# Performance work log

Measured on AMD Instinct MI355X. Metric: run time of the kernel, lower is better.

## Reference

```python
import jax, jax.numpy as jnp
import numpy as np

N_NODES = 100000
N_EDGES = 1600000
IN_CH = 64
HID = 64
OUT = 2


def sage_conv(x, src, dst, W_agg, W_root, b):
    # PyG SAGEConv (mean aggr): out = lin_l(mean_{j in N(i)} x_j) + lin_r(x_i)
    n = x.shape[0]
    msgs = x[src]                                        # [E, F] gather
    agg = jax.ops.segment_sum(msgs, dst, num_segments=n)  # [N, F] scatter-add
    cnt = jax.ops.segment_sum(jnp.ones((src.shape[0], 1), x.dtype), dst, num_segments=n)
    agg = agg / jnp.maximum(cnt, 1)                      # mean; isolated nodes -> 0
    return agg @ W_agg + x @ W_root + b


def setup_inputs() -> dict:
    key = jax.random.key(0)
    ks = jax.random.split(key, 8)
    s = lambda f: 1.0 / np.sqrt(f)
    x = jax.random.normal(ks[0], (N_NODES, IN_CH), dtype=jnp.float32)
    edge_index = jax.random.randint(ks[1], (2, N_EDGES), 0, N_NODES, dtype=jnp.int64)
    return {
        "x": x,
        "edge_index": edge_index,
        "W1_agg": jax.random.normal(ks[2], (IN_CH, HID), dtype=jnp.float32) * s(IN_CH),
        "W1_root": jax.random.normal(ks[3], (IN_CH, HID), dtype=jnp.float32) * s(IN_CH),
        "b1": jnp.zeros((HID,), jnp.float32),
        "W2_agg": jax.random.normal(ks[4], (HID, HID), dtype=jnp.float32) * s(HID),
        "W2_root": jax.random.normal(ks[5], (HID, HID), dtype=jnp.float32) * s(HID),
        "b2": jnp.zeros((HID,), jnp.float32),
        "W_lin": jax.random.normal(ks[6], (HID, OUT), dtype=jnp.float32) * s(HID),
        "b_lin": jnp.zeros((OUT,), jnp.float32),
    }


def reference(x, edge_index, W1_agg, W1_root, b1, W2_agg, W2_root, b2, W_lin, b_lin):
    src, dst = edge_index[0], edge_index[1]
    h = jax.nn.relu(sage_conv(x, src, dst, W1_agg, W1_root, b1))   # dropout = identity (eval)
    h = jax.nn.relu(sage_conv(h, src, dst, W2_agg, W2_root, b2))
    return h @ W_lin + b_lin
```

## Files before the change

kernel.cpp:

```cpp
#include <hip/hip_runtime.h>
#include <hip/hip_bf16.h>

#define FEAT 64
#define CHUNK 8192
#define MAX_NB 1024

typedef __attribute__((ext_vector_type(8))) short bf16x8;
typedef __attribute__((ext_vector_type(4))) float f32x4;
typedef __attribute__((ext_vector_type(2))) float f32x2;

__device__ __forceinline__ float bflo2f(unsigned int u) {
    union { unsigned int u; float f; } v; v.u = u << 16; return v.f;
}
__device__ __forceinline__ float bfhi2f(unsigned int u) {
    union { unsigned int u; float f; } v; v.u = u & 0xffff0000u; return v.f;
}
__device__ __forceinline__ unsigned short f2bf(float f) {
    union { float f; unsigned int u; } v; v.f = f;
    unsigned int u = v.u;
    u += 0x7fffu + ((u >> 16) & 1u);
    return (unsigned short)(u >> 16);
}
__device__ __forceinline__ f32x2 bfpair(unsigned int u) {
    f32x2 r; r.x = bflo2f(u & 0xffffu); r.y = bfhi2f(u); return r;
}

__global__ __launch_bounds__(256) void prep_kernel(
    const unsigned short* __restrict__ xh, const int* __restrict__ ei32,
    const void* __restrict__ w1a, const void* __restrict__ w1r,
    const void* __restrict__ b1,  const void* __restrict__ w2a,
    const void* __restrict__ w2r, const void* __restrict__ b2,
    const void* __restrict__ wl,  const void* __restrict__ bl,
    float* __restrict__ wbuf, unsigned short* __restrict__ Wt,
    int* __restrict__ flags, const void* __restrict__ x_in,
    unsigned short* __restrict__ x16, int n8) {
    __shared__ int cnt_bf, cnt_nz;
    int tid = threadIdx.x;
    if (tid == 0) { cnt_bf = 0; cnt_nz = 0; }
    __syncthreads();
    unsigned short h = xh[tid * 2];
    int e = (h >> 7) & 0xFF;
    if (e >= 110 && e <= 132) atomicAdd(&cnt_bf, 1);
    if (ei32[tid * 2 + 1] != 0) atomicAdd(&cnt_nz, 1);
    __syncthreads();
    int f0 = (cnt_bf >= 128) ? 1 : 0;
    if (blockIdx.x == 0 && tid == 0) {
        flags[0] = f0;
        flags[1] = (cnt_nz < 8) ? 1 : 0;
    }
    int i = blockIdx.x * 256 + tid;
    if (i < 16642) {
        const void* src; int off;
        if      (i < 4096)  { src = w1a; off = i; }
        else if (i < 8192)  { src = w1r; off = i - 4096; }
        else if (i < 8256)  { src = b1;  off = i - 8192; }
        else if (i < 12352) { src = w2a; off = i - 8256; }
        else if (i < 16448) { src = w2r; off = i - 12352; }
        else if (i < 16512) { src = b2;  off = i - 16448; }
        else if (i < 16640) { src = wl;  off = i - 16512; }
        else                { src = bl;  off = i - 16640; }
        float v = f0 ? bflo2f(((const unsigned short*)src)[off])
                     : ((const float*)src)[off];
        wbuf[i] = v;
        unsigned short hv = f2bf(v);
        if (i < 4096)                      Wt[(off & 63) * 128 + (off >> 6)] = hv;
        else if (i < 8192)                 Wt[(off & 63) * 128 + 64 + (off >> 6)] = hv;
        else if (i >= 8256 && i < 12352)   Wt[8192 + (off & 63) * 128 + (off >> 6)] = hv;
        else if (i >= 12352 && i < 16448)  Wt[8192 + (off & 63) * 128 + 64 + (off >> 6)] = hv;
    }
    if (!f0 && i < n8) {
        float4 a = ((const float4*)x_in)[2 * i];
        float4 b = ((const float4*)x_in)[2 * i + 1];
        uint4 o;
        o.x = (unsigned int)f2bf(a.x) | ((unsigned int)f2bf(a.y) << 16);
        o.y = (unsigned int)f2bf(a.z) | ((unsigned int)f2bf(a.w) << 16);
        o.z = (unsigned int)f2bf(b.x) | ((unsigned int)f2bf(b.y) << 16);
        o.w = (unsigned int)f2bf(b.z) | ((unsigned int)f2bf(b.w) << 16);
        ((uint4*)x16)[i] = o;
    }
}

__global__ __launch_bounds__(256) void p1_hist_kernel(
    const int* __restrict__ ei32, int* __restrict__ hist,
    int E, int N, int NB, int EC, const int* __restrict__ flags) {
    __shared__ int lh[MAX_NB];
    int tid = threadIdx.x, c = blockIdx.x;
    for (int i = tid; i < NB; i += 256) lh[i] = 0;
    __syncthreads();
    int idx64 = flags[1];
    long base = (long)c * CHUNK;
#pragma unroll 4
    for (int j = 0; j < CHUNK / 256; ++j) {
        long e = base + j * 256 + tid;
        if (e < E) {
            int d = idx64 ? ei32[2 * ((long)E + e)] : ei32[(long)E + e];
            if ((unsigned)d < (unsigned)N)
                atomicAdd(&lh[d >> 8], 1);
        }
    }
    __syncthreads();
    for (int k = tid; k < NB; k += 256) hist[(long)k * EC + c] = lh[k];
}

__global__ __launch_bounds__(256) void scan1_kernel(const int* __restrict__ in,
                                                    int* __restrict__ out,
                                                    int* __restrict__ blocksum, int n) {
    int tid = threadIdx.x;
    int base = blockIdx.x * 2048 + tid * 8;
    int v[8];
    int tsum = 0;
#pragma unroll
    for (int i = 0; i < 8; ++i) {
        v[i] = (base + i < n) ? in[base + i] : 0;
        tsum += v[i];
    }
    int lane = tid & 63;
    int x = tsum;
#pragma unroll
    for (int off = 1; off < 64; off <<= 1) {
        int y = __shfl_up(x, off);
        if (lane >= off) x += y;
    }
    __shared__ int wsum[4];
    int wave = tid >> 6;
    if (lane == 63) wsum[wave] = x;
    __syncthreads();
    int woff = 0;
#pragma unroll
    for (int w = 0; w < 4; ++w) if (w < wave) woff += wsum[w];
    int run = woff + x - tsum;
#pragma unroll
    for (int i = 0; i < 8; ++i) {
        if (base + i < n) out[base + i] = run;
        run += v[i];
    }
    if (tid == 255) blocksum[blockIdx.x] = woff + x;
}

__global__ void scan3_kernel(int* __restrict__ out, const int* __restrict__ blocksum, int n) {
    int i = blockIdx.x * 256 + threadIdx.x;
    if (i >= n) return;
    int nb = i >> 11;
    int pre = 0;
    for (int b = 0; b < nb; ++b) pre += blocksum[b];
    out[i] += pre;
}

__global__ __launch_bounds__(256) void p3_scatter_kernel(
    const int* __restrict__ ei32, const int* __restrict__ hscan,
    int* __restrict__ bkt, int E, int N, int NB, int EC,
    const int* __restrict__ flags) {
    __shared__ int lh[MAX_NB];
    int tid = threadIdx.x, c = blockIdx.x;
    for (int i = tid; i < NB; i += 256) lh[i] = 0;
    __syncthreads();
    int idx64 = flags[1];
    long base = (long)c * CHUNK;
#pragma unroll 4
    for (int j = 0; j < CHUNK / 256; ++j) {
        long e = base + j * 256 + tid;
        if (e < E) {
            int s = idx64 ? ei32[2 * e]             : ei32[e];
            int d = idx64 ? ei32[2 * ((long)E + e)] : ei32[(long)E + e];
            if ((unsigned)d < (unsigned)N) {
                if ((unsigned)s >= (unsigned)N) s = 0;
                int k = d >> 8;
                int r = atomicAdd(&lh[k], 1);
                bkt[hscan[(long)k * EC + c] + r] = s | ((d & 255) << 20);
            }
        }
    }
}

__global__ __launch_bounds__(256) void p4_build_kernel(
    const int* __restrict__ bkt, const int* __restrict__ hscan, const int* __restrict__ hist,
    int* __restrict__ offs, int* __restrict__ cnt, int* __restrict__ srcs,
    int E, int N, int NB, int EC) {
    int k = blockIdx.x, tid = threadIdx.x;
    int start = hscan[(long)k * EC];
    int end = (k + 1 < NB) ? hscan[(long)(k + 1) * EC]
                           : (hscan[(long)NB * EC - 1] + hist[(long)NB * EC - 1]);
    __shared__ int lc[256], lheads[256], wsum[4];
    lc[tid] = 0;
    __syncthreads();
    for (int e = start + tid; e < end; e += 256)
        atomicAdd(&lc[(bkt[e] >> 20) & 255], 1);
    __syncthreads();
    int cv = lc[tid];
    int lane = tid & 63, wave = tid >> 6;
    int x = cv;
#pragma unroll
    for (int off = 1; off < 64; off <<= 1) {
        int y = __shfl_up(x, off);
        if (lane >= off) x += y;
    }
    if (lane == 63) wsum[wave] = x;
    __syncthreads();
    int woff = 0;
#pragma unroll
    for (int w = 0; w < 4; ++w) if (w < wave) woff += wsum[w];
    int excl = woff + x - cv;
    int gnode = k * 256 + tid;
    if (gnode < N) { offs[gnode] = start + excl; cnt[gnode] = cv; }
    lheads[tid] = excl;
    __syncthreads();
    for (int e = start + tid; e < end; e += 256) {
        int p = bkt[e];
        int d8 = (p >> 20) & 255;
        int pos = start + atomicAdd(&lheads[d8], 1);
        srcs[pos] = p & 0xFFFFF;
    }
}

__global__ __launch_bounds__(256) void aggregate_kernel(
    const void* __restrict__ feat_raw, const unsigned short* __restrict__ feat_ws,
    const int* __restrict__ srcs,
    const int* __restrict__ offs, const int* __restrict__ cnt,
    unsigned short* __restrict__ agg16, int N, const int* __restrict__ flags) {
    const unsigned short* feat16 = flags[0] ? (const unsigned short*)feat_raw : feat_ws;
    int tid = threadIdx.x;
    int lane = tid & 63;
    int wave = tid >> 6;
    int g = lane >> 3;
    int li = lane & 7;
    int node = (blockIdx.x * 4 + wave) * 8 + g;
    if (node >= N) return;
    int start = offs[node];
    int deg = cnt[node];
    f32x2 a0 = {0.f, 0.f}, a1 = a0, a2 = a0, a3 = a0;
    int j = 0;
    for (; j + 4 <= deg; j += 4) {
        int s0 = srcs[start + j];
        int s1 = srcs[start + j + 1];
        int s2 = srcs[start + j + 2];
        int s3 = srcs[start + j + 3];
        uint4 u0 = *(const uint4*)(feat16 + (size_t)s0 * FEAT + 8 * li);
        uint4 u1 = *(const uint4*)(feat16 + (size_t)s1 * FEAT + 8 * li);
        uint4 u2 = *(const uint4*)(feat16 + (size_t)s2 * FEAT + 8 * li);
        uint4 u3 = *(const uint4*)(feat16 + (size_t)s3 * FEAT + 8 * li);
        a0 += bfpair(u0.x); a1 += bfpair(u0.y); a2 += bfpair(u0.z); a3 += bfpair(u0.w);
        a0 += bfpair(u1.x); a1 += bfpair(u1.y); a2 += bfpair(u1.z); a3 += bfpair(u1.w);
        a0 += bfpair(u2.x); a1 += bfpair(u2.y); a2 += bfpair(u2.z); a3 += bfpair(u2.w);
        a0 += bfpair(u3.x); a1 += bfpair(u3.y); a2 += bfpair(u3.z); a3 += bfpair(u3.w);
    }
    for (; j < deg; ++j) {
        int s = srcs[start + j];
        uint4 u = *(const uint4*)(feat16 + (size_t)s * FEAT + 8 * li);
        a0 += bfpair(u.x); a1 += bfpair(u.y); a2 += bfpair(u.z); a3 += bfpair(u.w);
    }
    float inv = 1.0f / (float)(deg > 0 ? deg : 1);
    uint4 o;
    o.x = (unsigned)f2bf(a0.x * inv) | ((unsigned)f2bf(a0.y * inv) << 16);
    o.y = (unsigned)f2bf(a1.x * inv) | ((unsigned)f2bf(a1.y * inv) << 16);
    o.z = (unsigned)f2bf(a2.x * inv) | ((unsigned)f2bf(a2.y * inv) << 16);
    o.w = (unsigned)f2bf(a3.x * inv) | ((unsigned)f2bf(a3.y * inv) << 16);
    *(uint4*)(agg16 + (size_t)node * FEAT + 8 * li) = o;
}

__global__ __launch_bounds__(256) void sage_gemm_kernel(
    const unsigned short* __restrict__ agg16,
    const void* __restrict__ root_raw, const unsigned short* __restrict__ root_ws,
    const unsigned short* __restrict__ Wt, const float* __restrict__ bias,
    unsigned short* __restrict__ out16, int N,
    const float* __restrict__ wl, const float* __restrict__ bl,
    void* __restrict__ out_final, const int* __restrict__ flags, int root_sel) {

    const unsigned short* root16 =
        (root_sel && !flags[0]) ? root_ws : (const unsigned short*)root_raw;

    __shared__ unsigned short A_l[64][136];
    __shared__ unsigned short B_l[64][136];

    int tid = threadIdx.x;
    int blk = blockIdx.x;

#pragma unroll
    for (int i = 0; i < 4; ++i) {
        int ch = tid + i * 256;
        int n = ch >> 4, kc = ch & 15;
        *(uint4*)&B_l[n][kc * 8] = *(const uint4*)(Wt + n * 128 + kc * 8);
    }
#pragma unroll
    for (int i = 0; i < 4; ++i) {
        int ch = tid + i * 256;
        int r = ch >> 4, c = ch & 15;
        int row = blk * 64 + r;
        uint4 u = make_uint4(0, 0, 0, 0);
        if (row < N)
            u = (c < 8) ? ((const uint4*)(agg16 + (size_t)row * FEAT))[c]
                        : ((const uint4*)(root16 + (size_t)row * FEAT))[c - 8];
        *(uint4*)&A_l[r][c * 8] = u;
    }
    __syncthreads();

    int lane = tid & 63;
    int wave = tid >> 6;
    int r0 = wave * 16;
    int m = lane & 15, quad = lane >> 4;

    f32x4 acc0 = {0.f, 0.f, 0.f, 0.f};
    f32x4 acc1 = acc0, acc2 = acc0, acc3 = acc0;

#pragma unroll
    for (int k0 = 0; k0 < 128; k0 += 32) {
        bf16x8 a = *(const bf16x8*)&A_l[r0 + m][k0 + quad * 8];
        bf16x8 b0 = *(const bf16x8*)&B_l[ 0 + m][k0 + quad * 8];
        bf16x8 b1 = *(const bf16x8*)&B_l[16 + m][k0 + quad * 8];
        bf16x8 b2 = *(const bf16x8*)&B_l[32 + m][k0 + quad * 8];
        bf16x8 b3 = *(const bf16x8*)&B_l[48 + m][k0 + quad * 8];
        acc0 = __builtin_amdgcn_mfma_f32_16x16x32_bf16(a, b0, acc0, 0, 0, 0);
        acc1 = __builtin_amdgcn_mfma_f32_16x16x32_bf16(a, b1, acc1, 0, 0, 0);
        acc2 = __builtin_amdgcn_mfma_f32_16x16x32_bf16(a, b2, acc2, 0, 0, 0);
        acc3 = __builtin_amdgcn_mfma_f32_16x16x32_bf16(a, b3, acc3, 0, 0, 0);
    }
    __syncthreads();

#pragma unroll
    for (int c = 0; c < 4; ++c) {
        f32x4 av = (c == 0) ? acc0 : (c == 1) ? acc1 : (c == 2) ? acc2 : acc3;
        float bv = bias[c * 16 + m];
#pragma unroll
        for (int reg = 0; reg < 4; ++reg) {
            float v = fmaxf(av[reg] + bv, 0.f);
            A_l[r0 + quad * 4 + reg][c * 16 + m] = f2bf(v);
        }
    }
    __syncthreads();

#pragma unroll
    for (int i = 0; i < 2; ++i) {
        int ch = tid + i * 256;
        int r = ch >> 3, c = ch & 7;
        int row = blk * 64 + r;
        if (row < N)
            ((uint4*)(out16 + (size_t)row * FEAT))[c] = *(const uint4*)&A_l[r][c * 8];
    }

    if (wl) {
        int r = tid >> 2, part = tid & 3;
        int row = blk * 64 + r;
        if (row < N) {
            float p0 = 0.f, p1 = 0.f;
#pragma unroll
            for (int j = 0; j < 16; ++j) {
                int f = part * 16 + j;
                float v = bflo2f(A_l[r][f]);
                p0 += v * wl[f * 2 + 0];
                p1 += v * wl[f * 2 + 1];
            }
            p0 += __shfl_down(p0, 2, 4); p0 += __shfl_down(p0, 1, 4);
            p1 += __shfl_down(p1, 2, 4); p1 += __shfl_down(p1, 1, 4);
            if (part == 0) {
                p0 += bl[0];
                p1 += bl[1];
                if (flags[0]) {
                    unsigned int o = ((unsigned int)f2bf(p1) << 16) | (unsigned int)f2bf(p0);
                    ((unsigned int*)out_final)[row] = o;
                } else {
                    ((float2*)out_final)[row] = make_float2(p0, p1);
                }
            }
        }
    }
}

extern "C" void kernel_launch(void* const* d_in, const int* in_sizes, int n_in,
                              void* d_out, int out_size, void* d_ws, size_t ws_size,
                              hipStream_t stream) {
    const void* x_in = d_in[0];
    const int*  ei32 = (const int*)d_in[1];

    int N = in_sizes[0] / FEAT;
    int E = in_sizes[1] / 2;
    int NB = (N + 255) >> 8;
    int EC = (E + CHUNK - 1) / CHUNK;
    int HN = NB * EC;

    unsigned short* x16   = (unsigned short*)d_ws;
    unsigned short* h16   = x16 + (size_t)N * FEAT;
    unsigned short* agg16 = h16 + (size_t)N * FEAT;
    unsigned short* Wt    = agg16 + (size_t)N * FEAT;
    float*          wbuf  = (float*)(Wt + 16384);
    int*            hist  = (int*)(wbuf + 16704);
    int*            hscan = hist + HN;
    int*            bsum  = hscan + HN;
    int*            flags = bsum + 1024;
    int*            offs  = flags + 16;
    int*            cnt   = offs + N;
    int*            bkt   = cnt + N;
    int*            srcs  = bkt + E;

    float* b1_32 = wbuf + 8192;
    float* b2_32 = wbuf + 16448;
    float* wl32  = wbuf + 16512;
    float* bl32  = wbuf + 16640;

    int n8 = N * FEAT / 8;
    int pBlocks = (n8 + 255) / 256;
    if (pBlocks < 66) pBlocks = 66;
    prep_kernel<<<pBlocks, 256, 0, stream>>>(
        (const unsigned short*)x_in, ei32,
        d_in[2], d_in[3], d_in[4], d_in[5], d_in[6], d_in[7], d_in[8], d_in[9],
        wbuf, Wt, flags, x_in, x16, n8);

    p1_hist_kernel<<<EC, 256, 0, stream>>>(ei32, hist, E, N, NB, EC, flags);
    int sB = (HN + 2047) / 2048;
    scan1_kernel<<<sB, 256, 0, stream>>>(hist, hscan, bsum, HN);
    scan3_kernel<<<(HN + 255) / 256, 256, 0, stream>>>(hscan, bsum, HN);
    p3_scatter_kernel<<<EC, 256, 0, stream>>>(ei32, hscan, bkt, E, N, NB, EC, flags);
    p4_build_kernel<<<NB, 256, 0, stream>>>(bkt, hscan, hist, offs, cnt, srcs, E, N, NB, EC);

    int aBlocks = (N + 31) / 32;
    int gBlocks = (N + 63) / 64;

    aggregate_kernel<<<aBlocks, 256, 0, stream>>>(x_in, x16, srcs, offs, cnt, agg16, N, flags);
    sage_gemm_kernel<<<gBlocks, 256, 0, stream>>>(agg16, x_in, x16, Wt, b1_32, h16, N,
                                                  nullptr, nullptr, nullptr, flags, 1);

    aggregate_kernel<<<aBlocks, 256, 0, stream>>>(h16, h16, srcs, offs, cnt, agg16, N, flags);
    sage_gemm_kernel<<<gBlocks, 256, 0, stream>>>(agg16, h16, h16, Wt + 8192, b2_32, h16, N,
                                                  wl32, bl32, d_out, flags, 0);
}
```

Measured before the change: 236.2 us.

## Fuse CSR build stages into one cooperative kernel with grid syncs

Replaces the six separate preprocessing launches (prep, histogram, two scans, scatter, build) with a single cooperative kernel that separates the phases with grid.sync(), falling back to the old launch sequence if the cooperative launch fails. It also halves the edge chunk size so more blocks share the histogram and scatter work, and skips writing the layer-2 hidden features since only the final linear output is needed. This targets per-launch overhead and small-grid tail effects, at the cost of running the scan and build phases on a grid capped at 512 blocks, which adds grid-wide barrier cost and less parallelism in the per-bucket build.

Measured after the change: 488.2 us. +106.7%, slower.

```diff
diff --git a/kernel.cpp b/kernel.cpp
--- a/kernel.cpp
+++ b/kernel.cpp
@@ -1,8 +1,11 @@
 #include <hip/hip_runtime.h>
 #include <hip/hip_bf16.h>
+#include <hip/hip_cooperative_groups.h>
+
+namespace cg = cooperative_groups;
 
 #define FEAT 64
-#define CHUNK 8192
+#define CHUNK 4096
 #define MAX_NB 1024
 
 typedef __attribute__((ext_vector_type(8))) short bf16x8;
@@ -23,6 +26,199 @@
 }
 __device__ __forceinline__ f32x2 bfpair(unsigned int u) {
     f32x2 r; r.x = bflo2f(u & 0xffffu); r.y = bfhi2f(u); return r;
+}
+
+__device__ __forceinline__ void weights_cvt_elem(
+    int i, int f0,
+    const void* w1a, const void* w1r, const void* b1, const void* w2a,
+    const void* w2r, const void* b2, const void* wl, const void* bl,
+    float* wbuf, unsigned short* Wt) {
+    const void* src; int off;
+    if      (i < 4096)  { src = w1a; off = i; }
+    else if (i < 8192)  { src = w1r; off = i - 4096; }
+    else if (i < 8256)  { src = b1;  off = i - 8192; }
+    else if (i < 12352) { src = w2a; off = i - 8256; }
+    else if (i < 16448) { src = w2r; off = i - 12352; }
+    else if (i < 16512) { src = b2;  off = i - 16448; }
+    else if (i < 16640) { src = wl;  off = i - 16512; }
+    else                { src = bl;  off = i - 16640; }
+    float v = f0 ? bflo2f(((const unsigned short*)src)[off])
+                 : ((const float*)src)[off];
+    wbuf[i] = v;
+    unsigned short hv = f2bf(v);
+    if (i < 4096)                      Wt[(off & 63) * 128 + (off >> 6)] = hv;
+    else if (i < 8192)                 Wt[(off & 63) * 128 + 64 + (off >> 6)] = hv;
+    else if (i >= 8256 && i < 12352)   Wt[8192 + (off & 63) * 128 + (off >> 6)] = hv;
+    else if (i >= 12352 && i < 16448)  Wt[8192 + (off & 63) * 128 + 64 + (off >> 6)] = hv;
+}
+
+__global__ __launch_bounds__(256) void coop_build_kernel(
+    const int* __restrict__ ei32, const void* __restrict__ x_in,
+    unsigned short* __restrict__ x16, int n8,
+    const void* __restrict__ w1a, const void* __restrict__ w1r,
+    const void* __restrict__ b1,  const void* __restrict__ w2a,
+    const void* __restrict__ w2r, const void* __restrict__ b2,
+    const void* __restrict__ wl,  const void* __restrict__ bl,
+    float* __restrict__ wbuf, unsigned short* __restrict__ Wt,
+    int* __restrict__ flags,
+    int* __restrict__ hist, int* __restrict__ hscan, int* __restrict__ bsum,
+    int* __restrict__ offs, int* __restrict__ cnt,
+    int* __restrict__ bkt, int* __restrict__ srcs,
+    int E, int N, int NB, int EC, int HN, int sB) {
+
+    cg::grid_group grid = cg::this_grid();
+    __shared__ int lh[MAX_NB];
+    __shared__ int lc[256], lheads[256], wsum[4];
+    __shared__ int s_cnt[2];
+
+    int tid = threadIdx.x;
+    int lane = tid & 63, wave = tid >> 6;
+
+    if (tid == 0) { s_cnt[0] = 0; s_cnt[1] = 0; }
+    __syncthreads();
+    {
+        const unsigned short* xh = (const unsigned short*)x_in;
+        unsigned short h = xh[tid * 2];
+        int e = (h >> 7) & 0xFF;
+        if (e >= 110 && e <= 132) atomicAdd(&s_cnt[0], 1);
+        if (ei32[tid * 2 + 1] != 0) atomicAdd(&s_cnt[1], 1);
+    }
+    __syncthreads();
+    int f0    = (s_cnt[0] >= 128) ? 1 : 0;
+    int idx64 = (s_cnt[1] < 8) ? 1 : 0;
+    if (blockIdx.x == 0 && tid == 0) { flags[0] = f0; flags[1] = idx64; }
+
+    for (int i = blockIdx.x * 256 + tid; i < 16642; i += gridDim.x * 256)
+        weights_cvt_elem(i, f0, w1a, w1r, b1, w2a, w2r, b2, wl, bl, wbuf, Wt);
+
+    if (!f0) {
+        for (int i = blockIdx.x * 256 + tid; i < n8; i += gridDim.x * 256) {
+            float4 a = ((const float4*)x_in)[2 * i];
+            float4 b = ((const float4*)x_in)[2 * i + 1];
+            uint4 o;
+            o.x = (unsigned int)f2bf(a.x) | ((unsigned int)f2bf(a.y) << 16);
+            o.y = (unsigned int)f2bf(a.z) | ((unsigned int)f2bf(a.w) << 16);
+            o.z = (unsigned int)f2bf(b.x) | ((unsigned int)f2bf(b.y) << 16);
+            o.w = (unsigned int)f2bf(b.z) | ((unsigned int)f2bf(b.w) << 16);
+            ((uint4*)x16)[i] = o;
+        }
+    }
+    grid.sync();
+
+    for (int c = blockIdx.x; c < EC; c += gridDim.x) {
+        for (int i = tid; i < NB; i += 256) lh[i] = 0;
+        __syncthreads();
+        long base = (long)c * CHUNK;
+#pragma unroll 4
+        for (int j = 0; j < CHUNK / 256; ++j) {
+            long e = base + j * 256 + tid;
+            if (e < E) {
+                int d = idx64 ? ei32[2 * ((long)E + e)] : ei32[(long)E + e];
+                if ((unsigned)d < (unsigned)N)
+                    atomicAdd(&lh[d >> 8], 1);
+            }
+        }
+        __syncthreads();
+        for (int k = tid; k < NB; k += 256) hist[(long)k * EC + c] = lh[k];
+        __syncthreads();
+    }
+    grid.sync();
+
+    for (int b = blockIdx.x; b < sB; b += gridDim.x) {
+        int base = b * 2048 + tid * 8;
+        int v[8];
+        int tsum = 0;
+#pragma unroll
+        for (int i = 0; i < 8; ++i) {
+            v[i] = (base + i < HN) ? hist[base + i] : 0;
+            tsum += v[i];
+        }
+        int x = tsum;
+#pragma unroll
+        for (int off = 1; off < 64; off <<= 1) {
+            int y = __shfl_up(x, off);
+            if (lane >= off) x += y;
+        }
+        if (lane == 63) wsum[wave] = x;
+        __syncthreads();
+        int woff = 0;
+#pragma unroll
+        for (int w = 0; w < 4; ++w) if (w < wave) woff += wsum[w];
+        int run = woff + x - tsum;
+#pragma unroll
+        for (int i = 0; i < 8; ++i) {
+            if (base + i < HN) hscan[base + i] = run;
+            run += v[i];
+        }
+        if (tid == 255) bsum[b] = woff + x;
+        __syncthreads();
+    }
+    grid.sync();
+
+    for (int i = blockIdx.x * 256 + tid; i < HN; i += gridDim.x * 256) {
+        int nb = i >> 11;
+        int pre = 0;
+        for (int b = 0; b < nb; ++b) pre += bsum[b];
+        hscan[i] += pre;
+    }
+    grid.sync();
+
+    for (int c = blockIdx.x; c < EC; c += gridDim.x) {
+        for (int i = tid; i < NB; i += 256) lh[i] = 0;
+        __syncthreads();
+        long base = (long)c * CHUNK;
+#pragma unroll 4
+        for (int j = 0; j < CHUNK / 256; ++j) {
+            long e = base + j * 256 + tid;
+            if (e < E) {
+                int s = idx64 ? ei32[2 * e]             : ei32[e];
+                int d = idx64 ? ei32[2 * ((long)E + e)] : ei32[(long)E + e];
+                if ((unsigned)d < (unsigned)N) {
+                    if ((unsigned)s >= (unsigned)N) s = 0;
+                    int k = d >> 8;
+                    int r = atomicAdd(&lh[k], 1);
+                    bkt[hscan[(long)k * EC + c] + r] = s | ((d & 255) << 20);
+                }
+            }
+        }
+        __syncthreads();
+    }
+    grid.sync();
+
+    for (int k = blockIdx.x; k < NB; k += gridDim.x) {
+        int start = hscan[(long)k * EC];
+        int end = (k + 1 < NB) ? hscan[(long)(k + 1) * EC]
+                               : (hscan[(long)NB * EC - 1] + hist[(long)NB * EC - 1]);
+        lc[tid] = 0;
+        __syncthreads();
+        for (int e = start + tid; e < end; e += 256)
+            atomicAdd(&lc[(bkt[e] >> 20) & 255], 1);
+        __syncthreads();
+        int cv = lc[tid];
+        int x = cv;
+#pragma unroll
+        for (int off = 1; off < 64; off <<= 1) {
+            int y = __shfl_up(x, off);
+            if (lane >= off) x += y;
+        }
+        if (lane == 63) wsum[wave] = x;
+        __syncthreads();
+        int woff = 0;
+#pragma unroll
+        for (int w = 0; w < 4; ++w) if (w < wave) woff += wsum[w];
+        int excl = woff + x - cv;
+        int gnode = k * 256 + tid;
+        if (gnode < N) { offs[gnode] = start + excl; cnt[gnode] = cv; }
+        lheads[tid] = excl;
+        __syncthreads();
+        for (int e = start + tid; e < end; e += 256) {
+            int p = bkt[e];
+            int d8 = (p >> 20) & 255;
+            int pos = start + atomicAdd(&lheads[d8], 1);
+            srcs[pos] = p & 0xFFFFF;
+        }
+        __syncthreads();
+    }
 }
 
 __global__ __launch_bounds__(256) void prep_kernel(
@@ -34,40 +230,23 @@
     float* __restrict__ wbuf, unsigned short* __restrict__ Wt,
     int* __restrict__ flags, const void* __restrict__ x_in,
     unsigned short* __restrict__ x16, int n8) {
-    __shared__ int cnt_bf, cnt_nz;
+    __shared__ int s_cnt[2];
     int tid = threadIdx.x;
-    if (tid == 0) { cnt_bf = 0; cnt_nz = 0; }
+    if (tid == 0) { s_cnt[0] = 0; s_cnt[1] = 0; }
     __syncthreads();
     unsigned short h = xh[tid * 2];
     int e = (h >> 7) & 0xFF;
-    if (e >= 110 && e <= 132) atomicAdd(&cnt_bf, 1);
-    if (ei32[tid * 2 + 1] != 0) atomicAdd(&cnt_nz, 1);
-    __syncthreads();
-    int f0 = (cnt_bf >= 128) ? 1 : 0;
+    if (e >= 110 && e <= 132) atomicAdd(&s_cnt[0], 1);
+    if (ei32[tid * 2 + 1] != 0) atomicAdd(&s_cnt[1], 1);
+    __syncthreads();
+    int f0 = (s_cnt[0] >= 128) ? 1 : 0;
     if (blockIdx.x == 0 && tid == 0) {
         flags[0] = f0;
-        flags[1] = (cnt_nz < 8) ? 1 : 0;
+        flags[1] = (s_cnt[1] < 8) ? 1 : 0;
     }
     int i = blockIdx.x * 256 + tid;
-    if (i < 16642) {
-        const void* src; int off;
-        if      (i < 4096)  { src = w1a; off = i; }
-        else if (i < 8192)  { src = w1r; off = i - 4096; }
-        else if (i < 8256)  { src = b1;  off = i - 8192; }
-        else if (i < 12352) { src = w2a; off = i - 8256; }
-        else if (i < 16448) { src = w2r; off = i - 12352; }
-        else if (i < 16512) { src = b2;  off = i - 16448; }
-        else if (i < 16640) { src = wl;  off = i - 16512; }
-        else                { src = bl;  off = i - 16640; }
-        float v = f0 ? bflo2f(((const unsigned short*)src)[off])
-                     : ((const float*)src)[off];
-        wbuf[i] = v;
-        unsigned short hv = f2bf(v);
-        if (i < 4096)                      Wt[(off & 63) * 128 + (off >> 6)] = hv;
-        else if (i < 8192)                 Wt[(off & 63) * 128 + 64 + (off >> 6)] = hv;
-        else if (i >= 8256 && i < 12352)   Wt[8192 + (off & 63) * 128 + (off >> 6)] = hv;
-        else if (i >= 12352 && i < 16448)  Wt[8192 + (off & 63) * 128 + 64 + (off >> 6)] = hv;
-    }
+    if (i < 16642)
+        weights_cvt_elem(i, f0, w1a, w1r, b1, w2a, w2r, b2, wl, bl, wbuf, Wt);
     if (!f0 && i < n8) {
         float4 a = ((const float4*)x_in)[2 * i];
         float4 b = ((const float4*)x_in)[2 * i + 1];
@@ -327,13 +506,15 @@
     }
     __syncthreads();
 
-#pragma unroll
-    for (int i = 0; i < 2; ++i) {
-        int ch = tid + i * 256;
-        int r = ch >> 3, c = ch & 7;
-        int row = blk * 64 + r;
-        if (row < N)
-            ((uint4*)(out16 + (size_t)row * FEAT))[c] = *(const uint4*)&A_l[r][c * 8];
+    if (out16) {
+#pragma unroll
+        for (int i = 0; i < 2; ++i) {
+            int ch = tid + i * 256;
+            int r = ch >> 3, c = ch & 7;
+            int row = blk * 64 + r;
+            if (row < N)
+                ((uint4*)(out16 + (size_t)row * FEAT))[c] = *(const uint4*)&A_l[r][c * 8];
+        }
     }
 
     if (wl) {
@@ -369,12 +550,17 @@
                               hipStream_t stream) {
     const void* x_in = d_in[0];
     const int*  ei32 = (const int*)d_in[1];
+    const void* w1a = d_in[2]; const void* w1r = d_in[3]; const void* b1 = d_in[4];
+    const void* w2a = d_in[5]; const void* w2r = d_in[6]; const void* b2 = d_in[7];
+    const void* wl  = d_in[8]; const void* bl  = d_in[9];
 
     int N = in_sizes[0] / FEAT;
     int E = in_sizes[1] / 2;
     int NB = (N + 255) >> 8;
     int EC = (E + CHUNK - 1) / CHUNK;
     int HN = NB * EC;
+    int sB = (HN + 2047) / 2048;
+    int n8 = N * FEAT / 8;
 
     unsigned short* x16   = (unsigned short*)d_ws;
     unsigned short* h16   = x16 + (size_t)N * FEAT;
@@ -395,20 +581,37 @@
     float* wl32  = wbuf + 16512;
     float* bl32  = wbuf + 16640;
 
-    int n8 = N * FEAT / 8;
-    int pBlocks = (n8 + 255) / 256;
-    if (pBlocks < 66) pBlocks = 66;
-    prep_kernel<<<pBlocks, 256, 0, stream>>>(
-        (const unsigned short*)x_in, ei32,
-        d_in[2], d_in[3], d_in[4], d_in[5], d_in[6], d_in[7], d_in[8], d_in[9],
-        wbuf, Wt, flags, x_in, x16, n8);
-
-    p1_hist_kernel<<<EC, 256, 0, stream>>>(ei32, hist, E, N, NB, EC, flags);
-    int sB = (HN + 2047) / 2048;
-    scan1_kernel<<<sB, 256, 0, stream>>>(hist, hscan, bsum, HN);
-    scan3_kernel<<<(HN + 255) / 256, 256, 0, stream>>>(hscan, bsum, HN);
-    p3_scatter_kernel<<<EC, 256, 0, stream>>>(ei32, hscan, bkt, E, N, NB, EC, flags);
-    p4_build_kernel<<<NB, 256, 0, stream>>>(bkt, hscan, hist, offs, cnt, srcs, E, N, NB, EC);
+    int gridB = NB > EC ? NB : EC;
+    if (gridB > 512) gridB = 512;
+    if (gridB < 64) gridB = 64;
+    {
+        const unsigned short* xh = (const unsigned short*)x_in;
+        void* args[] = {
+            (void*)&ei32, (void*)&x_in, (void*)&x16, (void*)&n8,
+            (void*)&w1a, (void*)&w1r, (void*)&b1, (void*)&w2a,
+            (void*)&w2r, (void*)&b2, (void*)&wl, (void*)&bl,
+            (void*)&wbuf, (void*)&Wt, (void*)&flags,
+            (void*)&hist, (void*)&hscan, (void*)&bsum,
+            (void*)&offs, (void*)&cnt, (void*)&bkt, (void*)&srcs,
+            (void*)&E, (void*)&N, (void*)&NB, (void*)&EC, (void*)&HN, (void*)&sB
+        };
+        hipError_t err = hipLaunchCooperativeKernel(
+            (void*)coop_build_kernel, dim3(gridB), dim3(256), args, 0, stream);
+        if (err != hipSuccess) {
+            (void)xh;
+            int pBlocks = (n8 + 255) / 256;
+            if (pBlocks < 66) pBlocks = 66;
+            prep_kernel<<<pBlocks, 256, 0, stream>>>(
+                (const unsigned short*)x_in, ei32,
+                w1a, w1r, b1, w2a, w2r, b2, wl, bl,
+                wbuf, Wt, flags, x_in, x16, n8);
+            p1_hist_kernel<<<EC, 256, 0, stream>>>(ei32, hist, E, N, NB, EC, flags);
+            scan1_kernel<<<sB, 256, 0, stream>>>(hist, hscan, bsum, HN);
+            scan3_kernel<<<(HN + 255) / 256, 256, 0, stream>>>(hscan, bsum, HN);
+            p3_scatter_kernel<<<EC, 256, 0, stream>>>(ei32, hscan, bkt, E, N, NB, EC, flags);
+            p4_build_kernel<<<NB, 256, 0, stream>>>(bkt, hscan, hist, offs, cnt, srcs, E, N, NB, EC);
+        }
+    }
 
     int aBlocks = (N + 31) / 32;
     int gBlocks = (N + 63) / 64;
@@ -418,6 +621,6 @@
                                                   nullptr, nullptr, nullptr, flags, 1);
 
     aggregate_kernel<<<aBlocks, 256, 0, stream>>>(h16, h16, srcs, offs, cnt, agg16, N, flags);
-    sage_gemm_kernel<<<gBlocks, 256, 0, stream>>>(agg16, h16, h16, Wt + 8192, b2_32, h16, N,
+    sage_gemm_kernel<<<gBlocks, 256, 0, stream>>>(agg16, h16, h16, Wt + 8192, b2_32, nullptr, N,
                                                   wl32, bl32, d_out, flags, 0);
 }
```
